# Kernel tuning notes

Hardware: AMD Instinct MI355X
Metric: run time of the kernel (lower is better)

## Reference

```python
import jax, jax.numpy as jnp
import numpy as np

N_HEADS = 16


def setup_inputs() -> dict:
    key = jax.random.key(0)
    ks = jax.random.split(key, 5)
    B, T, C = 4, 2048, 1024
    scale = 0.02
    return {
        "x": jax.random.normal(ks[0], (B, T, C), dtype=jnp.float32),
        "w_attn": jax.random.normal(ks[1], (C, 3 * C), dtype=jnp.float32) * scale,
        "b_attn": jax.random.normal(ks[2], (3 * C,), dtype=jnp.float32) * scale,
        "w_proj": jax.random.normal(ks[3], (C, C), dtype=jnp.float32) * scale,
        "b_proj": jax.random.normal(ks[4], (C,), dtype=jnp.float32) * scale,
    }


def reference(x, w_attn, b_attn, w_proj, b_proj):
    B, T, C = x.shape
    H = N_HEADS
    D = C // H  # head dim
    qkv = x @ w_attn + b_attn  # [B,T,3C]
    q, k, v = jnp.split(qkv, 3, axis=-1)
    # [B,T,C] -> [B,H,T,D]
    q = q.reshape(B, T, H, D).transpose(0, 2, 1, 3)
    k = k.reshape(B, T, H, D).transpose(0, 2, 1, 3)
    v = v.reshape(B, T, H, D).transpose(0, 2, 1, 3)
    att = jnp.einsum("bhtd,bhsd->bhts", q, k) * (1.0 / jnp.sqrt(jnp.float32(D)))
    causal = jnp.tril(jnp.ones((T, T), dtype=bool))  # [T,T]
    att = jnp.where(causal[None, None], att, -jnp.inf)
    att = jax.nn.softmax(att, axis=-1)
    y = jnp.einsum("bhts,bhsd->bhtd", att, v)  # [B,H,T,D]
    y = y.transpose(0, 2, 1, 3).reshape(B, T, C)
    return y @ w_proj + b_proj
```

## Files before the change

kernel.cpp:

```cpp
#include <hip/hip_runtime.h>
#include <hip/hip_bf16.h>
#include <math.h>

typedef __attribute__((ext_vector_type(8))) short short8;
typedef __attribute__((ext_vector_type(4))) short short4v;
typedef __attribute__((ext_vector_type(4))) float f32x4;
typedef __attribute__((ext_vector_type(2))) unsigned int uint2v;
typedef unsigned int u32;

#define MFMA16(a, b, c) __builtin_amdgcn_mfma_f32_16x16x16bf16_1k(a, b, c, 0, 0, 0)
#define MFMA32(a, b, c) __builtin_amdgcn_mfma_f32_16x16x32_bf16(a, b, c, 0, 0, 0)

#define GLB(p) ((const __attribute__((address_space(1))) u32*)(p))
#define LDS(p) ((__attribute__((address_space(3))) u32*)(p))

#define QSCALE 0.18033688011111204f

#define KV_STRIDE 72
#define KV_TILE 4608
#define KV_CHUNK 9216

__device__ __forceinline__ unsigned short f2bf(float f) {
  unsigned int u = __float_as_uint(f);
  u += 0x7fffu + ((u >> 16) & 1u);
  return (unsigned short)(u >> 16);
}


__global__ __launch_bounds__(256) void cvt_bf16(const float* __restrict__ in,
                                                unsigned short* __restrict__ out, int n4) {
  int i = blockIdx.x * blockDim.x + threadIdx.x;
  if (i < n4) {
    float4 f = ((const float4*)in)[i];
    ushort4 o;
    o.x = f2bf(f.x); o.y = f2bf(f.y); o.z = f2bf(f.z); o.w = f2bf(f.w);
    ((ushort4*)out)[i] = o;
  }
}

__global__ __launch_bounds__(256) void transpose_cvt(const float* __restrict__ in,
                                                     unsigned short* __restrict__ out,
                                                     int R, int C) {
  __shared__ float tile[32][33];
  int bx = blockIdx.x * 32;
  int by = blockIdx.y * 32;
  int tx = threadIdx.x, ty = threadIdx.y;
#pragma unroll
  for (int i = 0; i < 32; i += 8)
    tile[ty + i][tx] = in[(size_t)(by + ty + i) * C + bx + tx];
  __syncthreads();
#pragma unroll
  for (int i = 0; i < 32; i += 8)
    out[(size_t)(bx + ty + i) * R + by + tx] = f2bf(tile[tx][ty + i]);
}


template <int MODE>
__global__ __launch_bounds__(256)
void gemm_bt(const unsigned short* __restrict__ A, const unsigned short* __restrict__ Bt,
             const float* __restrict__ bias, float* __restrict__ outf,
             unsigned short* __restrict__ q_ws, unsigned short* __restrict__ kv_ws,
             int M, int N, int K) {
  __shared__ unsigned short As[128 * 32];
  __shared__ unsigned short Bs[128 * 32];
  const int tid = threadIdx.x;
  const int wid = tid >> 6;
  const int lane = tid & 63;
  const int quad = lane >> 4;
  const int l15 = lane & 15;
  const int m0 = blockIdx.x * 128;
  const int n0 = blockIdx.y * 128;
  const int wm = (wid >> 1) * 64;
  const int wn = (wid & 1) * 64;

  const int srow = wid * 32 + (lane >> 2);
  const int scol = (lane & 3) * 8;
  const unsigned short* ga0 = A + (size_t)(m0 + srow) * K + scol;
  const unsigned short* ga1 = ga0 + (size_t)16 * K;
  const unsigned short* gb0 = Bt + (size_t)(n0 + srow) * K + scol;
  const unsigned short* gb1 = gb0 + (size_t)16 * K;
  unsigned short* la0 = As + srow * 32 + scol;
  unsigned short* la1 = la0 + 16 * 32;
  unsigned short* lb0 = Bs + srow * 32 + scol;
  unsigned short* lb1 = lb0 + 16 * 32;

  f32x4 acc[4][4];
#pragma unroll
  for (int i = 0; i < 4; i++)
#pragma unroll
    for (int j = 0; j < 4; j++) acc[i][j] = (f32x4){0.f, 0.f, 0.f, 0.f};

  for (int k0 = 0; k0 < K; k0 += 32) {
    __builtin_amdgcn_global_load_lds(GLB(ga0 + k0), LDS(la0), 16, 0, 0);
    __builtin_amdgcn_global_load_lds(GLB(ga1 + k0), LDS(la1), 16, 0, 0);
    __builtin_amdgcn_global_load_lds(GLB(gb0 + k0), LDS(lb0), 16, 0, 0);
    __builtin_amdgcn_global_load_lds(GLB(gb1 + k0), LDS(lb1), 16, 0, 0);
    __syncthreads();
    short8 af[4], bf[4];
#pragma unroll
    for (int i = 0; i < 4; i++)
      af[i] = *(const short8*)(As + (wm + i * 16 + l15) * 32 + quad * 8);
#pragma unroll
    for (int j = 0; j < 4; j++)
      bf[j] = *(const short8*)(Bs + (wn + j * 16 + l15) * 32 + quad * 8);
#pragma unroll
    for (int i = 0; i < 4; i++)
#pragma unroll
      for (int j = 0; j < 4; j++)
        acc[i][j] = MFMA32(af[i], bf[j], acc[i][j]);
    __syncthreads();
  }

  const int colbase = n0 + wn;
  const int which = colbase >> 10;

  if (MODE == 0) {
    const int h = (colbase & 1023) >> 6;
    if (which == 2) {
#pragma unroll
      for (int j = 0; j < 4; j++) {
        const float bv = bias[colbase + j * 16 + l15];
        const int d = j * 16 + l15;
#pragma unroll
        for (int i = 0; i < 4; i++) {
          const int t = m0 + wm + i * 16 + quad * 4;
          const int b = t >> 11;
          const int tt = t & 2047;
          ushort4 pv;
          pv.x = f2bf(acc[i][j][0] + bv);
          pv.y = f2bf(acc[i][j][1] + bv);
          pv.z = f2bf(acc[i][j][2] + bv);
          pv.w = f2bf(acc[i][j][3] + bv);
          const size_t cbase = ((size_t)((b * 16 + h) * 32) + (tt >> 6)) * KV_CHUNK + KV_TILE;
          *(ushort4*)(&kv_ws[cbase + (size_t)d * KV_STRIDE + (tt & 63)]) = pv;
        }
      }
    } else {
      short4v idf;
#pragma unroll
      for (int j4 = 0; j4 < 4; j4++)
        idf[j4] = (quad * 4 + j4 == l15) ? (short)0x3F80 : (short)0;
#pragma unroll
      for (int j = 0; j < 4; j++) {
        const float bv = bias[colbase + j * 16 + l15];
#pragma unroll
        for (int i = 0; i < 4; i++) {
          short4v pf;
          if (which == 0) {
#pragma unroll
            for (int r = 0; r < 4; r++) pf[r] = (short)f2bf((acc[i][j][r] + bv) * QSCALE);
          } else {
#pragma unroll
            for (int r = 0; r < 4; r++) pf[r] = (short)f2bf(acc[i][j][r] + bv);
          }
          f32x4 dt = MFMA16(pf, idf, ((f32x4){0.f, 0.f, 0.f, 0.f}));
          const int t = m0 + wm + i * 16 + l15;
          const int b = t >> 11;
          const int tt = t & 2047;
          const int dd = j * 16 + quad * 4;
          ushort4 qv;
          qv.x = f2bf(dt[0]);
          qv.y = f2bf(dt[1]);
          qv.z = f2bf(dt[2]);
          qv.w = f2bf(dt[3]);
          if (which == 0) {
            *(ushort4*)(&q_ws[(((size_t)((b * 16 + h) * 2048) + tt) * 64) + dd]) = qv;
          } else {
            const size_t cbase = ((size_t)((b * 16 + h) * 32) + (tt >> 6)) * KV_CHUNK;
            *(ushort4*)(&kv_ws[cbase + (size_t)(tt & 63) * KV_STRIDE + dd]) = qv;
          }
        }
      }
    }
  } else {
#pragma unroll
    for (int j = 0; j < 4; j++) {
      const int col = colbase + j * 16 + l15;
      const float bv = bias[col];
#pragma unroll
      for (int i = 0; i < 4; i++) {
#pragma unroll
        for (int r = 0; r < 4; r++) {
          const int row = m0 + wm + i * 16 + quad * 4 + r;
          outf[(size_t)row * N + col] = acc[i][j][r] + bv;
        }
      }
    }
  }
}


__global__ __launch_bounds__(256)
void attn_fwd(const unsigned short* __restrict__ q_ws, const unsigned short* __restrict__ kv_ws,
              unsigned short* __restrict__ y_ws) {
  __shared__ unsigned short KV[2][KV_CHUNK];
  const int tid = threadIdx.x;
  const int w = tid >> 6;
  const int lane = tid & 63;
  const int quad = lane >> 4;
  const int l15 = lane & 15;
  const int ip = blockIdx.x;
  const int bh = blockIdx.y;
  const unsigned short* Qp = q_ws + (size_t)bh * 2048 * 64;
  const unsigned short* KVp = kv_ws + (size_t)bh * 32 * KV_CHUNK;

  int qT[4];
  qT[0] = ip * 64 + w * 16;
  qT[1] = (15 - ip) * 64 + w * 16;
  qT[2] = (16 + ip) * 64 + w * 16;
  qT[3] = (31 - ip) * 64 + w * 16;

  short8 qfr[4][2];
#pragma unroll
  for (int f = 0; f < 4; f++)
#pragma unroll
    for (int c = 0; c < 2; c++)
      qfr[f][c] = *(const short8*)(Qp + (size_t)(qT[f] + l15) * 64 + c * 32 + quad * 8);

  f32x4 o[4][4];
#pragma unroll
  for (int f = 0; f < 4; f++)
#pragma unroll
    for (int db = 0; db < 4; db++) o[f][db] = (f32x4){0.f, 0.f, 0.f, 0.f};
  float lsum[4] = {0.f, 0.f, 0.f, 0.f};

  const int nch = 32 - ip;

  for (int i = w; i < 18; i += 4)
    __builtin_amdgcn_global_load_lds(GLB(KVp + i * 512 + lane * 8),
                                     LDS(&KV[0][i * 512 + lane * 8]), 16, 0, 0);

  for (int c = 0; c < nch; c++) {
    __syncthreads();
    const int buf = c & 1;
    if (c + 1 < nch) {
      const unsigned short* src = KVp + (size_t)(c + 1) * KV_CHUNK;
      for (int i = w; i < 18; i += 4)
        __builtin_amdgcn_global_load_lds(GLB(src + i * 512 + lane * 8),
                                         LDS(&KV[buf ^ 1][i * 512 + lane * 8]), 16, 0, 0);
    }
    const unsigned short* Ksb = KV[buf];
    const unsigned short* Vtb = KV[buf] + KV_TILE;
    const int kbase = c * 64;

#pragma unroll
    for (int tb = 0; tb < 2; tb++) {
      const int kb = kbase + tb * 32;
      if (kb > qT[3] + 15) break;
      const int kloc = tb * 32;
      short8 kf[2][2];
#pragma unroll
      for (int t2 = 0; t2 < 2; t2++)
#pragma unroll
        for (int cc = 0; cc < 2; cc++)
          kf[t2][cc] =
              *(const short8*)(&Ksb[(kloc + t2 * 16 + l15) * KV_STRIDE + cc * 32 + quad * 8]);
      short4v vf[2][4];
#pragma unroll
      for (int t2 = 0; t2 < 2; t2++)
#pragma unroll
        for (int db = 0; db < 4; db++)
          vf[t2][db] =
              *(const short4v*)(&Vtb[(db * 16 + l15) * KV_STRIDE + kloc + t2 * 16 + quad * 4]);

#pragma unroll
      for (int f = 0; f < 4; f++) {
        const int qf0 = qT[f];
        if (kb > qf0 + 15) continue;
        f32x4 s0 = (f32x4){0.f, 0.f, 0.f, 0.f};
        f32x4 s1 = (f32x4){0.f, 0.f, 0.f, 0.f};
        s0 = MFMA32(kf[0][0], qfr[f][0], s0);
        s0 = MFMA32(kf[0][1], qfr[f][1], s0);
        s1 = MFMA32(kf[1][0], qfr[f][0], s1);
        s1 = MFMA32(kf[1][1], qfr[f][1], s1);
        const int qg = qf0 + l15;
        if (kb + 31 > qf0) {
#pragma unroll
          for (int r = 0; r < 4; r++) {
            if (kb + quad * 4 + r > qg) s0[r] = -INFINITY;
            if (kb + 16 + quad * 4 + r > qg) s1[r] = -INFINITY;
          }
        }
        float p[8];
#pragma unroll
        for (int r = 0; r < 4; r++) {
          p[r] = __builtin_amdgcn_exp2f(s0[r]);
          p[4 + r] = __builtin_amdgcn_exp2f(s1[r]);
        }
        lsum[f] += ((p[0] + p[1]) + (p[2] + p[3])) + ((p[4] + p[5]) + (p[6] + p[7]));
        u32 u[8];
#pragma unroll
        for (int i = 0; i < 8; i++) u[i] = __float_as_uint(p[i]) + 0x8000u;
        uint2v t0, t1;
        t0.x = __builtin_amdgcn_perm(u[1], u[0], 0x07060302u);
        t0.y = __builtin_amdgcn_perm(u[3], u[2], 0x07060302u);
        t1.x = __builtin_amdgcn_perm(u[5], u[4], 0x07060302u);
        t1.y = __builtin_amdgcn_perm(u[7], u[6], 0x07060302u);
        short4v pf0 = __builtin_bit_cast(short4v, t0);
        short4v pf1 = __builtin_bit_cast(short4v, t1);
#pragma unroll
        for (int db = 0; db < 4; db++) {
          o[f][db] = MFMA16(vf[0][db], pf0, o[f][db]);
          o[f][db] = MFMA16(vf[1][db], pf1, o[f][db]);
        }
      }
    }
  }

  const int b = bh >> 4, h = bh & 15;
#pragma unroll
  for (int f = 0; f < 4; f++) {
    float ls = lsum[f];
    ls += __shfl_xor(ls, 16);
    ls += __shfl_xor(ls, 32);
    const int qg = qT[f] + l15;
    const float inv = 1.0f / ls;
    const size_t rowoff = ((size_t)(b * 2048 + qg)) * 1024 + h * 64;
#pragma unroll
    for (int db = 0; db < 4; db++) {
      ushort4 ov;
      ov.x = f2bf(o[f][db][0] * inv);
      ov.y = f2bf(o[f][db][1] * inv);
      ov.z = f2bf(o[f][db][2] * inv);
      ov.w = f2bf(o[f][db][3] * inv);
      *(ushort4*)(y_ws + rowoff + db * 16 + quad * 4) = ov;
    }
  }
}


extern "C" void kernel_launch(void* const* d_in, const int* in_sizes, int n_in,
                              void* d_out, int out_size, void* d_ws, size_t ws_size,
                              hipStream_t stream) {
  const float* x = (const float*)d_in[0];
  const float* w_attn = (const float*)d_in[1];
  const float* b_attn = (const float*)d_in[2];
  const float* w_proj = (const float*)d_in[3];
  const float* b_proj = (const float*)d_in[4];
  float* out = (float*)d_out;

  unsigned short* xb = (unsigned short*)d_ws;
  unsigned short* wat = xb + (size_t)8192 * 1024;
  unsigned short* wpt = wat + (size_t)3072 * 1024;
  unsigned short* q_ws = wpt + (size_t)1024 * 1024;
  unsigned short* kv_ws = q_ws + (size_t)8388608;
  unsigned short* y_ws = xb;

  cvt_bf16<<<8192, 256, 0, stream>>>(x, xb, 2097152);
  transpose_cvt<<<dim3(96, 32), dim3(32, 8), 0, stream>>>(w_attn, wat, 1024, 3072);
  transpose_cvt<<<dim3(32, 32), dim3(32, 8), 0, stream>>>(w_proj, wpt, 1024, 1024);

  gemm_bt<0><<<dim3(64, 24), 256, 0, stream>>>(xb, wat, b_attn, nullptr, q_ws, kv_ws,
                                               8192, 3072, 1024);
  attn_fwd<<<dim3(8, 64), 256, 0, stream>>>(q_ws, kv_ws, y_ws);
  gemm_bt<1><<<dim3(64, 8), 256, 0, stream>>>(y_ws, wpt, b_proj, out, nullptr, nullptr,
                                              8192, 1024, 1024);
}
```

Measured before the change: 274.3 us.

## Replace GEMMs with 256x256 double-buffered, swizzled, XCD-remapped MFMA kernel

```diff
diff --git a/kernel.cpp b/kernel.cpp
--- a/kernel.cpp
+++ b/kernel.cpp
@@ -55,63 +55,162 @@
 }
 
 
+#define AH 16384
+#define BUFH 32768
+
 template <int MODE>
-__global__ __launch_bounds__(256)
-void gemm_bt(const unsigned short* __restrict__ A, const unsigned short* __restrict__ Bt,
+__global__ __launch_bounds__(512, 2)
+void gemm256(const unsigned short* __restrict__ A, const unsigned short* __restrict__ Bt,
              const float* __restrict__ bias, float* __restrict__ outf,
              unsigned short* __restrict__ q_ws, unsigned short* __restrict__ kv_ws,
              int M, int N, int K) {
-  __shared__ unsigned short As[128 * 32];
-  __shared__ unsigned short Bs[128 * 32];
+  __shared__ unsigned short sm[2 * BUFH];
   const int tid = threadIdx.x;
   const int wid = tid >> 6;
   const int lane = tid & 63;
   const int quad = lane >> 4;
   const int l15 = lane & 15;
-  const int m0 = blockIdx.x * 128;
-  const int n0 = blockIdx.y * 128;
-  const int wm = (wid >> 1) * 64;
-  const int wn = (wid & 1) * 64;
-
-  const int srow = wid * 32 + (lane >> 2);
-  const int scol = (lane & 3) * 8;
-  const unsigned short* ga0 = A + (size_t)(m0 + srow) * K + scol;
-  const unsigned short* ga1 = ga0 + (size_t)16 * K;
-  const unsigned short* gb0 = Bt + (size_t)(n0 + srow) * K + scol;
-  const unsigned short* gb1 = gb0 + (size_t)16 * K;
-  unsigned short* la0 = As + srow * 32 + scol;
-  unsigned short* la1 = la0 + 16 * 32;
-  unsigned short* lb0 = Bs + srow * 32 + scol;
-  unsigned short* lb1 = lb0 + 16 * 32;
-
-  f32x4 acc[4][4];
-#pragma unroll
-  for (int i = 0; i < 4; i++)
+  const int wrow = (wid >> 2) * 128;
+  const int wn = wid & 3;
+
+  const int NB = N >> 8;
+  const int nwg = (M >> 8) * NB;
+  const int cpx = nwg >> 3;
+  const int wg = ((int)blockIdx.x & 7) * cpx + ((int)blockIdx.x >> 3);
+  const int m0 = (wg / NB) << 8;
+  const int n0 = (wg % NB) << 8;
+
+  const int trow = tid >> 3;
+  const int tcol = tid & 7;
+  const unsigned short* gA = A + (size_t)(m0 + trow) * K + ((tcol ^ (trow & 7)) << 3);
+  const unsigned short* gB = Bt + (size_t)(n0 + trow) * K + ((tcol ^ (trow & 7)) << 3);
+  const int ldsA = trow * 64 + tcol * 8;
+  const int ldsB = ldsA + AH;
+
+  const int sw0 = ((quad) ^ (l15 & 7)) * 8;
+  const int sw1 = ((quad + 4) ^ (l15 & 7)) * 8;
+  const int aRow = wrow * 64 + l15 * 64;
+  const int bRow = AH + wn * 4096 + l15 * 64;
+
+#define SA(buf, kt, g)                                                          \
+  __builtin_amdgcn_global_load_lds(GLB(gA + (size_t)((g) * 64) * K + (kt) * 64), \
+                                   LDS(sm + (buf) * BUFH + ldsA + (g) * 4096), 16, 0, 0)
+#define SB(buf, kt, h)                                                          \
+  __builtin_amdgcn_global_load_lds(GLB(gB + (size_t)((h) * 64) * K + (kt) * 64), \
+                                   LDS(sm + (buf) * BUFH + ldsB + (h) * 4096), 16, 0, 0)
+#define RA(d, buf, rf, s) d = *(const short8*)(sm + (buf) * BUFH + aRow + (rf) * 1024 + (s))
+#define RB(d, buf, cf, s) d = *(const short8*)(sm + (buf) * BUFH + bRow + (cf) * 1024 + (s))
+#define MF4(i, a, B0, B1, B2, B3)       \
+  acc[i][0] = MFMA32(a, B0, acc[i][0]); \
+  acc[i][1] = MFMA32(a, B1, acc[i][1]); \
+  acc[i][2] = MFMA32(a, B2, acc[i][2]); \
+  acc[i][3] = MFMA32(a, B3, acc[i][3])
+#define PHASE_TAIL()                                 \
+  __builtin_amdgcn_s_barrier();                      \
+  asm volatile("s_waitcnt lgkmcnt(0)" ::: "memory"); \
+  __builtin_amdgcn_sched_barrier(0);                 \
+  __builtin_amdgcn_s_setprio(1)
+#define PHASE_END()             \
+  __builtin_amdgcn_s_setprio(0); \
+  __builtin_amdgcn_s_barrier()
+
+  f32x4 acc[8][4];
+#pragma unroll
+  for (int i = 0; i < 8; i++)
 #pragma unroll
     for (int j = 0; j < 4; j++) acc[i][j] = (f32x4){0.f, 0.f, 0.f, 0.f};
 
-  for (int k0 = 0; k0 < K; k0 += 32) {
-    __builtin_amdgcn_global_load_lds(GLB(ga0 + k0), LDS(la0), 16, 0, 0);
-    __builtin_amdgcn_global_load_lds(GLB(ga1 + k0), LDS(la1), 16, 0, 0);
-    __builtin_amdgcn_global_load_lds(GLB(gb0 + k0), LDS(lb0), 16, 0, 0);
-    __builtin_amdgcn_global_load_lds(GLB(gb1 + k0), LDS(lb1), 16, 0, 0);
-    __syncthreads();
-    short8 af[4], bf[4];
-#pragma unroll
-    for (int i = 0; i < 4; i++)
-      af[i] = *(const short8*)(As + (wm + i * 16 + l15) * 32 + quad * 8);
-#pragma unroll
-    for (int j = 0; j < 4; j++)
-      bf[j] = *(const short8*)(Bs + (wn + j * 16 + l15) * 32 + quad * 8);
-#pragma unroll
-    for (int i = 0; i < 4; i++)
-#pragma unroll
-      for (int j = 0; j < 4; j++)
-        acc[i][j] = MFMA32(af[i], bf[j], acc[i][j]);
-    __syncthreads();
+  const int T = K >> 6;
+  const int U = T >> 1;
+
+  SB(0, 0, 0); SB(0, 0, 1); SB(0, 0, 2); SB(0, 0, 3);
+  SA(0, 0, 0); SA(0, 0, 1); SA(0, 0, 2); SA(0, 0, 3);
+  SB(1, 1, 0); SB(1, 1, 1); SB(1, 1, 2); SB(1, 1, 3);
+  asm volatile("s_waitcnt vmcnt(4)" ::: "memory");
+  __builtin_amdgcn_s_barrier();
+
+  short8 a0, a1, a2, a3, b00, b01, b02, b03, b10, b11, b12, b13;
+
+  for (int u = 0; u < U; ++u) {
+    const int t1 = 2 * u + 1;
+    const int t2 = 2 * u + 2;
+    const bool more = (u + 1 < U);
+    RA(a0, 0, 0, sw0); RA(a1, 0, 1, sw0); RA(a2, 0, 2, sw0); RA(a3, 0, 3, sw0);
+    RB(b00, 0, 0, sw0); RB(b01, 0, 1, sw0); RB(b02, 0, 2, sw0); RB(b03, 0, 3, sw0);
+    SA(1, t1, 0); SA(1, t1, 2);
+    PHASE_TAIL();
+    MF4(0, a0, b00, b01, b02, b03);
+    MF4(1, a1, b00, b01, b02, b03);
+    MF4(2, a2, b00, b01, b02, b03);
+    MF4(3, a3, b00, b01, b02, b03);
+    PHASE_END();
+    RA(a0, 0, 0, sw1); RA(a1, 0, 1, sw1); RA(a2, 0, 2, sw1); RA(a3, 0, 3, sw1);
+    RB(b10, 0, 0, sw1); RB(b11, 0, 1, sw1); RB(b12, 0, 2, sw1); RB(b13, 0, 3, sw1);
+    SA(1, t1, 1); SA(1, t1, 3);
+    PHASE_TAIL();
+    MF4(0, a0, b10, b11, b12, b13);
+    MF4(1, a1, b10, b11, b12, b13);
+    MF4(2, a2, b10, b11, b12, b13);
+    MF4(3, a3, b10, b11, b12, b13);
+    PHASE_END();
+    RA(a0, 0, 4, sw0); RA(a1, 0, 5, sw0); RA(a2, 0, 6, sw0); RA(a3, 0, 7, sw0);
+    if (more) { SB(0, t2, 0); SB(0, t2, 1); }
+    PHASE_TAIL();
+    MF4(4, a0, b00, b01, b02, b03);
+    MF4(5, a1, b00, b01, b02, b03);
+    MF4(6, a2, b00, b01, b02, b03);
+    MF4(7, a3, b00, b01, b02, b03);
+    PHASE_END();
+    RA(a0, 0, 4, sw1); RA(a1, 0, 5, sw1); RA(a2, 0, 6, sw1); RA(a3, 0, 7, sw1);
+    if (more) { SB(0, t2, 2); SB(0, t2, 3); }
+    PHASE_TAIL();
+    MF4(4, a0, b10, b11, b12, b13);
+    MF4(5, a1, b10, b11, b12, b13);
+    MF4(6, a2, b10, b11, b12, b13);
+    MF4(7, a3, b10, b11, b12, b13);
+    __builtin_amdgcn_s_setprio(0);
+    if (more) { asm volatile("s_waitcnt vmcnt(4)" ::: "memory"); }
+    else      { asm volatile("s_waitcnt vmcnt(0)" ::: "memory"); }
+    __builtin_amdgcn_s_barrier();
+    RA(a0, 1, 0, sw0); RA(a1, 1, 1, sw0); RA(a2, 1, 2, sw0); RA(a3, 1, 3, sw0);
+    RB(b00, 1, 0, sw0); RB(b01, 1, 1, sw0); RB(b02, 1, 2, sw0); RB(b03, 1, 3, sw0);
+    if (more) { SA(0, t2, 0); SA(0, t2, 2); }
+    PHASE_TAIL();
+    MF4(0, a0, b00, b01, b02, b03);
+    MF4(1, a1, b00, b01, b02, b03);
+    MF4(2, a2, b00, b01, b02, b03);
+    MF4(3, a3, b00, b01, b02, b03);
+    PHASE_END();
+    RA(a0, 1, 0, sw1); RA(a1, 1, 1, sw1); RA(a2, 1, 2, sw1); RA(a3, 1, 3, sw1);
+    RB(b10, 1, 0, sw1); RB(b11, 1, 1, sw1); RB(b12, 1, 2, sw1); RB(b13, 1, 3, sw1);
+    if (more) { SA(0, t2, 1); SA(0, t2, 3); }
+    PHASE_TAIL();
+    MF4(0, a0, b10, b11, b12, b13);
+    MF4(1, a1, b10, b11, b12, b13);
+    MF4(2, a2, b10, b11, b12, b13);
+    MF4(3, a3, b10, b11, b12, b13);
+    PHASE_END();
+    RA(a0, 1, 4, sw0); RA(a1, 1, 5, sw0); RA(a2, 1, 6, sw0); RA(a3, 1, 7, sw0);
+    if (more) { SB(1, t2 + 1, 0); SB(1, t2 + 1, 1); }
+    PHASE_TAIL();
+    MF4(4, a0, b00, b01, b02, b03);
+    MF4(5, a1, b00, b01, b02, b03);
+    MF4(6, a2, b00, b01, b02, b03);
+    MF4(7, a3, b00, b01, b02, b03);
+    PHASE_END();
+    RA(a0, 1, 4, sw1); RA(a1, 1, 5, sw1); RA(a2, 1, 6, sw1); RA(a3, 1, 7, sw1);
+    if (more) { SB(1, t2 + 1, 2); SB(1, t2 + 1, 3); }
+    PHASE_TAIL();
+    MF4(4, a0, b10, b11, b12, b13);
+    MF4(5, a1, b10, b11, b12, b13);
+    MF4(6, a2, b10, b11, b12, b13);
+    MF4(7, a3, b10, b11, b12, b13);
+    __builtin_amdgcn_s_setprio(0);
+    if (more) { asm volatile("s_waitcnt vmcnt(4)" ::: "memory"); }
+    __builtin_amdgcn_s_barrier();
   }
 
-  const int colbase = n0 + wn;
+  const int colbase = n0 + wn * 64;
   const int which = colbase >> 10;
 
   if (MODE == 0) {
@@ -122,8 +221,8 @@
         const float bv = bias[colbase + j * 16 + l15];
         const int d = j * 16 + l15;
 #pragma unroll
-        for (int i = 0; i < 4; i++) {
-          const int t = m0 + wm + i * 16 + quad * 4;
+        for (int i = 0; i < 8; i++) {
+          const int t = m0 + wrow + i * 16 + quad * 4;
           const int b = t >> 11;
           const int tt = t & 2047;
           ushort4 pv;
@@ -144,7 +243,7 @@
       for (int j = 0; j < 4; j++) {
         const float bv = bias[colbase + j * 16 + l15];
 #pragma unroll
-        for (int i = 0; i < 4; i++) {
+        for (int i = 0; i < 8; i++) {
           short4v pf;
           if (which == 0) {
 #pragma unroll
@@ -154,7 +253,7 @@
             for (int r = 0; r < 4; r++) pf[r] = (short)f2bf(acc[i][j][r] + bv);
           }
           f32x4 dt = MFMA16(pf, idf, ((f32x4){0.f, 0.f, 0.f, 0.f}));
-          const int t = m0 + wm + i * 16 + l15;
+          const int t = m0 + wrow + i * 16 + l15;
           const int b = t >> 11;
           const int tt = t & 2047;
           const int dd = j * 16 + quad * 4;
@@ -178,15 +277,22 @@
       const int col = colbase + j * 16 + l15;
       const float bv = bias[col];
 #pragma unroll
-      for (int i = 0; i < 4; i++) {
+      for (int i = 0; i < 8; i++) {
 #pragma unroll
         for (int r = 0; r < 4; r++) {
-          const int row = m0 + wm + i * 16 + quad * 4 + r;
+          const int row = m0 + wrow + i * 16 + quad * 4 + r;
           outf[(size_t)row * N + col] = acc[i][j][r] + bv;
         }
       }
     }
   }
+#undef SA
+#undef SB
+#undef RA
+#undef RB
+#undef MF4
+#undef PHASE_TAIL
+#undef PHASE_END
 }
 
 
@@ -350,9 +456,9 @@
   transpose_cvt<<<dim3(96, 32), dim3(32, 8), 0, stream>>>(w_attn, wat, 1024, 3072);
   transpose_cvt<<<dim3(32, 32), dim3(32, 8), 0, stream>>>(w_proj, wpt, 1024, 1024);
 
-  gemm_bt<0><<<dim3(64, 24), 256, 0, stream>>>(xb, wat, b_attn, nullptr, q_ws, kv_ws,
-                                               8192, 3072, 1024);
+  gemm256<0><<<dim3(384), dim3(512), 0, stream>>>(xb, wat, b_attn, nullptr, q_ws, kv_ws,
+                                                  8192, 3072, 1024);
   attn_fwd<<<dim3(8, 64), 256, 0, stream>>>(q_ws, kv_ws, y_ws);
-  gemm_bt<1><<<dim3(64, 8), 256, 0, stream>>>(y_ws, wpt, b_proj, out, nullptr, nullptr,
-                                              8192, 1024, 1024);
-}
+  gemm256<1><<<dim3(128), dim3(512), 0, stream>>>(y_ws, wpt, b_proj, out, nullptr, nullptr,
+                                                  8192, 1024, 1024);
+}
```

Result: slower. 281.7 us (+2.7%).

## Replace GEMM kernels with multi-buffered, swizzled, XCD-remapped pipelined GEMM

Applied to the files above, without the earlier changes.

```diff
diff --git a/kernel.cpp b/kernel.cpp
--- a/kernel.cpp
+++ b/kernel.cpp
@@ -55,63 +55,164 @@
 }
 
 
-template <int MODE>
-__global__ __launch_bounds__(256)
-void gemm_bt(const unsigned short* __restrict__ A, const unsigned short* __restrict__ Bt,
-             const float* __restrict__ bias, float* __restrict__ outf,
-             unsigned short* __restrict__ q_ws, unsigned short* __restrict__ kv_ws,
-             int M, int N, int K) {
-  __shared__ unsigned short As[128 * 32];
-  __shared__ unsigned short Bs[128 * 32];
+template <int MODE, int NWAVES, int RF>
+__global__ __launch_bounds__(NWAVES * 64, (RF == 8) ? 4 : 2)
+void gemm_p(const unsigned short* __restrict__ A, const unsigned short* __restrict__ Bt,
+            const float* __restrict__ bias, float* __restrict__ outf,
+            unsigned short* __restrict__ q_ws, unsigned short* __restrict__ kv_ws,
+            int M, int N, int K) {
+  constexpr int NW_N = NWAVES / 2;
+  constexpr int BM = RF * 32;
+  constexpr int BN = NW_N * 64;
+  constexpr int THREADS = NWAVES * 64;
+  constexpr int ATILE = BM * 32;
+  constexpr int BTILE = BN * 32;
+  constexpr int SWH = THREADS * 8;
+  constexpr int SWROWS = THREADS / 4;
+  __shared__ unsigned short sm[2 * ATILE + 3 * BTILE];
+
   const int tid = threadIdx.x;
   const int wid = tid >> 6;
   const int lane = tid & 63;
   const int quad = lane >> 4;
   const int l15 = lane & 15;
-  const int m0 = blockIdx.x * 128;
-  const int n0 = blockIdx.y * 128;
-  const int wm = (wid >> 1) * 64;
-  const int wn = (wid & 1) * 64;
-
-  const int srow = wid * 32 + (lane >> 2);
-  const int scol = (lane & 3) * 8;
-  const unsigned short* ga0 = A + (size_t)(m0 + srow) * K + scol;
-  const unsigned short* ga1 = ga0 + (size_t)16 * K;
-  const unsigned short* gb0 = Bt + (size_t)(n0 + srow) * K + scol;
-  const unsigned short* gb1 = gb0 + (size_t)16 * K;
-  unsigned short* la0 = As + srow * 32 + scol;
-  unsigned short* la1 = la0 + 16 * 32;
-  unsigned short* lb0 = Bs + srow * 32 + scol;
-  unsigned short* lb1 = lb0 + 16 * 32;
-
-  f32x4 acc[4][4];
-#pragma unroll
-  for (int i = 0; i < 4; i++)
+  const int wr = wid / NW_N;
+  const int wn = wid % NW_N;
+
+  const int NB = N / BN;
+  const int nwg = (M / BM) * NB;
+  const int cpx = nwg >> 3;
+  const int wg = ((int)blockIdx.x & 7) * cpx + ((int)blockIdx.x >> 3);
+  const int m0 = (wg / NB) * BM;
+  const int n0 = (wg % NB) * BN;
+
+  const int so = (tid & 7) ^ ((tid >> 3) & 7);
+  const int grow = 2 * (tid >> 3) + (so >> 2);
+  const int gcol = (so & 3) * 8;
+  const unsigned short* gAs = A + (size_t)(m0 + grow) * K + gcol;
+  const unsigned short* gBs = Bt + (size_t)(n0 + grow) * K + gcol;
+  const int ldst = tid * 8;
+
+  const int sA = ((4 * (l15 & 1) + quad) ^ (l15 >> 1)) * 8;
+  const int aLane = (wr * (RF * 8) + (l15 >> 1)) * 64 + sA;
+  const int bLane = (wn * 32 + (l15 >> 1)) * 64 + sA;
+
+  int bRd0 = 2 * ATILE + bLane;
+  int bRd1 = bRd0 + BTILE;
+  int bRd2 = bRd1 + BTILE;
+  int bSt0 = 2 * ATILE + ldst;
+  int bSt1 = bSt0 + BTILE;
+  int bSt2 = bSt1 + BTILE;
+
+#define SA(ab, kt)                                                                     \
+  do {                                                                                 \
+    __builtin_amdgcn_global_load_lds(GLB(gAs + (size_t)(kt) * 32),                     \
+                                     LDS(sm + (ab) * ATILE + ldst), 16, 0, 0);         \
+    __builtin_amdgcn_global_load_lds(GLB(gAs + (size_t)SWROWS * K + (size_t)(kt) * 32),\
+                                     LDS(sm + (ab) * ATILE + SWH + ldst), 16, 0, 0);   \
+  } while (0)
+#define SBr(dst, kt)                                                                   \
+  do {                                                                                 \
+    __builtin_amdgcn_global_load_lds(GLB(gBs + (size_t)(kt) * 32),                     \
+                                     LDS(sm + (dst)), 16, 0, 0);                       \
+    __builtin_amdgcn_global_load_lds(GLB(gBs + (size_t)SWROWS * K + (size_t)(kt) * 32),\
+                                     LDS(sm + (dst) + SWH), 16, 0, 0);                 \
+  } while (0)
+#define RA(d, ab, rf) d = *(const short8*)(sm + (ab) * ATILE + aLane + (rf) * 512)
+#define RB(d, rd, cf) d = *(const short8*)(sm + (rd) + (cf) * 512)
+#define MF4(i, a)                         \
+  acc[i][0] = MFMA32(a, b0, acc[i][0]);   \
+  acc[i][1] = MFMA32(a, b1, acc[i][1]);   \
+  acc[i][2] = MFMA32(a, b2, acc[i][2]);   \
+  acc[i][3] = MFMA32(a, b3, acc[i][3])
+#define TAILB()                                      \
+  __builtin_amdgcn_s_barrier();                      \
+  asm volatile("s_waitcnt lgkmcnt(0)" ::: "memory"); \
+  __builtin_amdgcn_sched_barrier(0);                 \
+  __builtin_amdgcn_s_setprio(1)
+#define ENDB()                   \
+  __builtin_amdgcn_s_setprio(0); \
+  __builtin_amdgcn_s_barrier()
+#define ROT()                                      \
+  do {                                             \
+    int _t = bRd0; bRd0 = bRd1; bRd1 = bRd2; bRd2 = _t; \
+    _t = bSt0; bSt0 = bSt1; bSt1 = bSt2; bSt2 = _t;     \
+  } while (0)
+#define VM(n) asm volatile("s_waitcnt vmcnt(" #n ")" ::: "memory")
+
+  f32x4 acc[RF][4];
+#pragma unroll
+  for (int i = 0; i < RF; i++)
 #pragma unroll
     for (int j = 0; j < 4; j++) acc[i][j] = (f32x4){0.f, 0.f, 0.f, 0.f};
 
-  for (int k0 = 0; k0 < K; k0 += 32) {
-    __builtin_amdgcn_global_load_lds(GLB(ga0 + k0), LDS(la0), 16, 0, 0);
-    __builtin_amdgcn_global_load_lds(GLB(ga1 + k0), LDS(la1), 16, 0, 0);
-    __builtin_amdgcn_global_load_lds(GLB(gb0 + k0), LDS(lb0), 16, 0, 0);
-    __builtin_amdgcn_global_load_lds(GLB(gb1 + k0), LDS(lb1), 16, 0, 0);
-    __syncthreads();
-    short8 af[4], bf[4];
-#pragma unroll
-    for (int i = 0; i < 4; i++)
-      af[i] = *(const short8*)(As + (wm + i * 16 + l15) * 32 + quad * 8);
-#pragma unroll
-    for (int j = 0; j < 4; j++)
-      bf[j] = *(const short8*)(Bs + (wn + j * 16 + l15) * 32 + quad * 8);
-#pragma unroll
-    for (int i = 0; i < 4; i++)
-#pragma unroll
-      for (int j = 0; j < 4; j++)
-        acc[i][j] = MFMA32(af[i], bf[j], acc[i][j]);
-    __syncthreads();
+  const int T = K >> 5;
+  short8 a0, a1, a2, a3, b0, b1, b2, b3;
+
+  if constexpr (RF == 8) {
+    SA(0, 0); SBr(bSt0, 0); SBr(bSt1, 1); SBr(bSt2, 2);
+    VM(4);
+    __builtin_amdgcn_s_barrier();
+    for (int t = 0; t < T; t += 2) {
+      RA(a0, 0, 0); RA(a1, 0, 1); RA(a2, 0, 2); RA(a3, 0, 3);
+      RB(b0, bRd0, 0); RB(b1, bRd0, 1); RB(b2, bRd0, 2); RB(b3, bRd0, 3);
+      if (t + 1 < T) SA(1, t + 1);
+      TAILB();
+      MF4(0, a0); MF4(1, a1); MF4(2, a2); MF4(3, a3);
+      ENDB();
+      RA(a0, 0, 4); RA(a1, 0, 5); RA(a2, 0, 6); RA(a3, 0, 7);
+      if (t + 3 < T) SBr(bSt0, t + 3);
+      TAILB();
+      MF4(4, a0); MF4(5, a1); MF4(6, a2); MF4(7, a3);
+      __builtin_amdgcn_s_setprio(0);
+      if (t + 1 < T) { if (t + 3 < T) { VM(2); } else { VM(0); } }
+      __builtin_amdgcn_s_barrier();
+      ROT();
+      RA(a0, 1, 0); RA(a1, 1, 1); RA(a2, 1, 2); RA(a3, 1, 3);
+      RB(b0, bRd0, 0); RB(b1, bRd0, 1); RB(b2, bRd0, 2); RB(b3, bRd0, 3);
+      if (t + 2 < T) SA(0, t + 2);
+      TAILB();
+      MF4(0, a0); MF4(1, a1); MF4(2, a2); MF4(3, a3);
+      ENDB();
+      RA(a0, 1, 4); RA(a1, 1, 5); RA(a2, 1, 6); RA(a3, 1, 7);
+      if (t + 4 < T) SBr(bSt0, t + 4);
+      TAILB();
+      MF4(4, a0); MF4(5, a1); MF4(6, a2); MF4(7, a3);
+      __builtin_amdgcn_s_setprio(0);
+      if (t + 2 < T) { if (t + 4 < T) { VM(2); } else { VM(0); } }
+      __builtin_amdgcn_s_barrier();
+      ROT();
+    }
+  } else {
+    SA(0, 0); SBr(bSt0, 0); SBr(bSt1, 1);
+    VM(2);
+    __builtin_amdgcn_s_barrier();
+    for (int t = 0; t < T; t += 2) {
+      RA(a0, 0, 0); RA(a1, 0, 1); RA(a2, 0, 2); RA(a3, 0, 3);
+      RB(b0, bRd0, 0); RB(b1, bRd0, 1); RB(b2, bRd0, 2); RB(b3, bRd0, 3);
+      if (t + 1 < T) SA(1, t + 1);
+      if (t + 2 < T) SBr(bSt2, t + 2);
+      TAILB();
+      MF4(0, a0); MF4(1, a1); MF4(2, a2); MF4(3, a3);
+      __builtin_amdgcn_s_setprio(0);
+      if (t + 1 < T) { if (t + 2 < T) { VM(2); } else { VM(0); } }
+      __builtin_amdgcn_s_barrier();
+      ROT();
+      RA(a0, 1, 0); RA(a1, 1, 1); RA(a2, 1, 2); RA(a3, 1, 3);
+      RB(b0, bRd0, 0); RB(b1, bRd0, 1); RB(b2, bRd0, 2); RB(b3, bRd0, 3);
+      if (t + 2 < T) SA(0, t + 2);
+      if (t + 3 < T) SBr(bSt2, t + 3);
+      TAILB();
+      MF4(0, a0); MF4(1, a1); MF4(2, a2); MF4(3, a3);
+      __builtin_amdgcn_s_setprio(0);
+      if (t + 2 < T) { if (t + 3 < T) { VM(2); } else { VM(0); } }
+      __builtin_amdgcn_s_barrier();
+      ROT();
+    }
   }
 
-  const int colbase = n0 + wn;
+  const int wrow = wr * (RF * 16);
+  const int colbase = n0 + wn * 64;
   const int which = colbase >> 10;
 
   if (MODE == 0) {
@@ -122,8 +223,8 @@
         const float bv = bias[colbase + j * 16 + l15];
         const int d = j * 16 + l15;
 #pragma unroll
-        for (int i = 0; i < 4; i++) {
-          const int t = m0 + wm + i * 16 + quad * 4;
+        for (int i = 0; i < RF; i++) {
+          const int t = m0 + wrow + i * 16 + quad * 4;
           const int b = t >> 11;
           const int tt = t & 2047;
           ushort4 pv;
@@ -144,7 +245,7 @@
       for (int j = 0; j < 4; j++) {
         const float bv = bias[colbase + j * 16 + l15];
 #pragma unroll
-        for (int i = 0; i < 4; i++) {
+        for (int i = 0; i < RF; i++) {
           short4v pf;
           if (which == 0) {
 #pragma unroll
@@ -154,7 +255,7 @@
             for (int r = 0; r < 4; r++) pf[r] = (short)f2bf(acc[i][j][r] + bv);
           }
           f32x4 dt = MFMA16(pf, idf, ((f32x4){0.f, 0.f, 0.f, 0.f}));
-          const int t = m0 + wm + i * 16 + l15;
+          const int t = m0 + wrow + i * 16 + l15;
           const int b = t >> 11;
           const int tt = t & 2047;
           const int dd = j * 16 + quad * 4;
@@ -178,15 +279,24 @@
       const int col = colbase + j * 16 + l15;
       const float bv = bias[col];
 #pragma unroll
-      for (int i = 0; i < 4; i++) {
+      for (int i = 0; i < RF; i++) {
 #pragma unroll
         for (int r = 0; r < 4; r++) {
-          const int row = m0 + wm + i * 16 + quad * 4 + r;
+          const int row = m0 + wrow + i * 16 + quad * 4 + r;
           outf[(size_t)row * N + col] = acc[i][j][r] + bv;
         }
       }
     }
   }
+#undef SA
+#undef SBr
+#undef RA
+#undef RB
+#undef MF4
+#undef TAILB
+#undef ENDB
+#undef ROT
+#undef VM
 }
 
 
@@ -350,9 +460,9 @@
   transpose_cvt<<<dim3(96, 32), dim3(32, 8), 0, stream>>>(w_attn, wat, 1024, 3072);
   transpose_cvt<<<dim3(32, 32), dim3(32, 8), 0, stream>>>(w_proj, wpt, 1024, 1024);
 
-  gemm_bt<0><<<dim3(64, 24), 256, 0, stream>>>(xb, wat, b_attn, nullptr, q_ws, kv_ws,
-                                               8192, 3072, 1024);
+  gemm_p<0, 8, 8><<<dim3(384), dim3(512), 0, stream>>>(xb, wat, b_attn, nullptr, q_ws, kv_ws,
+                                                       8192, 3072, 1024);
   attn_fwd<<<dim3(8, 64), 256, 0, stream>>>(q_ws, kv_ws, y_ws);
-  gemm_bt<1><<<dim3(64, 8), 256, 0, stream>>>(y_ws, wpt, b_proj, out, nullptr, nullptr,
-                                              8192, 1024, 1024);
-}
+  gemm_p<1, 4, 4><<<dim3(512), dim3(256), 0, stream>>>(y_ws, wpt, b_proj, out, nullptr, nullptr,
+                                                       8192, 1024, 1024);
+}
```

Result: slower. 800.4 us (+191.7%).
